# Optimization experiments

Measured on AMD Instinct MI355X. Metric: run time of the kernel, lower is better.

## Reference

```python
import jax, jax.numpy as jnp
import numpy as np

N = 10000        # num_nodes
F_IN = 256       # dataset_num_features
H = 128          # hidden_channels
C_OUT = 40       # dataset_num_classes
L = 3            # num_layers
HEADS = 8
DH = H // HEADS  # per-head dim
E = 160000       # num edges (before self loops)
SCALE = 1.0 / float(np.sqrt(DH))


def setup_inputs() -> dict:
    key = jax.random.key(0)
    ks = jax.random.split(key, 8)
    s = lambda k, *sh: (jax.random.normal(k, sh, dtype=jnp.float32) * 0.05)
    return dict(
        edge_index=jax.random.randint(ks[0], (2, E), 0, N, dtype=jnp.int32),
        x_param=s(ks[1], N, F_IN),
        lin1_w=s(ks[2], F_IN, H),
        lin1_b=jnp.zeros((H,), jnp.float32),
        wq=s(ks[3], L, H, H),
        wk=s(ks[4], L, H, H),
        wv=s(ks[5], L, H, H),
        bq=jnp.zeros((L, H), jnp.float32),
        bk=jnp.zeros((L, H), jnp.float32),
        bv=jnp.zeros((L, H), jnp.float32),
        lin2_w=s(ks[6], H, C_OUT),
        lin2_b=jnp.zeros((C_OUT,), jnp.float32),
    )


def _gcn_norm(edge_index):
    # PyG gcn_norm: add self loops (weight 1), symmetric D^-1/2 A D^-1/2
    loops = jnp.arange(N, dtype=edge_index.dtype)
    row = jnp.concatenate([edge_index[0], loops])  # source j
    col = jnp.concatenate([edge_index[1], loops])  # target i
    deg = jax.ops.segment_sum(jnp.ones(row.shape, jnp.float32), col, num_segments=N)
    dis = jnp.where(deg > 0, jax.lax.rsqrt(jnp.maximum(deg, 1e-12)), 0.0)
    return row, col, dis[row] * dis[col]


def _restricted_softmax(score):
    # softmax with an implicit extra logit at `margin=0`
    m = jnp.maximum(jnp.max(score, axis=-1, keepdims=True), 0.0)
    e = jnp.exp(score - m)
    return e / (jnp.sum(e, axis=-1, keepdims=True) + jnp.exp(-m))


def _forward(edge_index, x_param, lin1_w, lin1_b, wq, wk, wv, bq, bk, bv, lin2_w, lin2_b):
    row, col, norm = _gcn_norm(edge_index)
    # dropouts are eval-mode no-ops
    x = jax.nn.relu(x_param @ lin1_w + lin1_b)  # [N, H]
    x_all = x[:, None, :]                       # [N, 1, H]
    for l in range(L):
        t = x_all.shape[1]
        # project per-node first (linear commutes with per-edge gather)
        q = (x_all[:, -1] @ wq[l] + bq[l]).reshape(N, HEADS, DH)      # query from latest state
        k = (x_all @ wk[l] + bk[l]).reshape(N, t, HEADS, DH)          # keys over full history
        v = (x_all @ wv[l] + bv[l]).reshape(N, t, HEADS, DH)
        qe = q[col]   # [Etot, heads, dh]   (x_i)
        ke = k[row]   # [Etot, t, heads, dh] (x_j)
        ve = v[row]
        score = jnp.einsum('ehd,ethd->eht', qe, ke) * SCALE
        attn = _restricted_softmax(score)        # attention-dropout is a no-op in eval
        msg = jnp.einsum('eht,ethd->ehd', attn, ve).reshape(-1, H) * norm[:, None]
        out = jax.ops.segment_sum(msg, col, num_segments=N)  # aggr='add'
        x = jax.nn.relu(out)
        x_all = jnp.concatenate([x_all, x[:, None, :]], axis=1)
    logits = x_all[:, -1] @ lin2_w + lin2_b
    return jax.nn.log_softmax(logits, axis=1)


def reference(edge_index, x_param, lin1_w, lin1_b, wq, wk, wv, bq, bk, bv, lin2_w, lin2_b):
    return _forward(edge_index, x_param, lin1_w, lin1_b, wq, wk, wv, bq, bk, bv, lin2_w, lin2_b)
```

## Files before the change

kernel.cpp:

```cpp
#include <hip/hip_runtime.h>
#include <math.h>

#define N_NODES 10000
#define F_IN_D  256
#define H_DIM   128
#define C_OUTD  40
#define NHEADS  8
#define NEDGES  160000
#define ETOT    (NEDGES + N_NODES)
#define SCALE_F 0.25f
#define TILES_N 157

typedef __attribute__((ext_vector_type(8))) short bf16x8;
typedef __attribute__((ext_vector_type(4))) float f32x4;
typedef __attribute__((ext_vector_type(2))) float f32x2;

__device__ __forceinline__ unsigned short f2bf(float f) {
    unsigned int u = __float_as_uint(f);
    unsigned int r = (u + 0x7FFFu + ((u >> 16) & 1u)) >> 16;
    return (unsigned short)r;
}
__device__ __forceinline__ float bf2f(unsigned short h) {
    return __uint_as_float(((unsigned int)h) << 16);
}
__device__ __forceinline__ unsigned char f2fp8(float v) {
    int pk = __builtin_amdgcn_cvt_pk_fp8_f32(v, v, 0, false);
    return (unsigned char)(pk & 0xff);
}


__global__ void k_deg_count(const int* __restrict__ col, int* degi) {
    int e = blockIdx.x * 256 + threadIdx.x;
    if (e < NEDGES) atomicAdd(&degi[col[e]], 1);
}

__global__ void k_scan(const int* __restrict__ degi, int* offsets, int* cursor) {
    __shared__ int part[256];
    int tid = threadIdx.x;
    int s = 0;
    if (tid < 250) {
        const int4* d4 = (const int4*)degi;
        for (int i = 0; i < 10; ++i) {
            int4 v = d4[tid * 10 + i];
            s += v.x + v.y + v.z + v.w;
        }
    }
    part[tid] = s;
    __syncthreads();
    for (int off = 1; off < 256; off <<= 1) {
        int v = 0;
        if (tid >= off) v = part[tid - off];
        __syncthreads();
        part[tid] += v;
        __syncthreads();
    }
    if (tid < 250) {
        int base = part[tid] - s;
        int beg = tid * 40;
        for (int i = 0; i < 40; ++i) {
            offsets[beg + i] = base;
            cursor[beg + i]  = 0;
            base += degi[beg + i];
        }
    }
}

__global__ void k_scatter(const int* __restrict__ row, const int* __restrict__ col,
                          const int* __restrict__ degi, const int* __restrict__ offsets,
                          int* cursor, int* csr_row, float* csr_norm) {
    int e = blockIdx.x * 256 + threadIdx.x;
    if (e >= ETOT) return;
    int r, c;
    if (e < NEDGES) { r = row[e]; c = col[e]; }
    else            { r = c = e - NEDGES; }
    int slot = offsets[c] + atomicAdd(&cursor[c], 1);
    float dr = rsqrtf((float)degi[r]);
    float dc = rsqrtf((float)degi[c]);
    csr_row[slot]  = r;
    csr_norm[slot] = dr * dc;
}


__global__ void k_prep(const float* __restrict__ w1, const float* __restrict__ wq,
                       const float* __restrict__ wk, const float* __restrict__ wv,
                       const float* __restrict__ w2,
                       unsigned short* __restrict__ W1T, unsigned short* __restrict__ WTq,
                       unsigned short* __restrict__ WTk, unsigned short* __restrict__ WTv,
                       unsigned short* __restrict__ W2T, int* __restrict__ degi) {
    int b = blockIdx.x;
    if (b < 728) {
        int e = b * 256 + threadIdx.x;
        if (e < 32768) {
            int n = e >> 8, k = e & 255;
            W1T[e] = f2bf(w1[k * H_DIM + n]);
        } else if (e < 180224) {
            int e2 = e - 32768;
            int mat = e2 >> 14;
            int r   = e2 & 16383;
            int n = r >> 7, k = r & 127;
            int l = mat / 3, ws = mat % 3;
            const float*    src = (ws == 0) ? wq  : (ws == 1) ? wk  : wv;
            unsigned short* dst = (ws == 0) ? WTq : (ws == 1) ? WTk : WTv;
            dst[l * 16384 + n * H_DIM + k] = f2bf(src[l * 16384 + k * H_DIM + n]);
        } else if (e < 186368) {
            int e3 = e - 180224;
            int c = e3 >> 7, k = e3 & 127;
            W2T[c * H_DIM + k] = (c < C_OUTD) ? f2bf(w2[k * C_OUTD + c]) : 0;
        }
    } else {
        int i = (b - 728) * 256 + threadIdx.x;
        if (i < N_NODES) degi[i] = 1;
    }
}


__global__ __launch_bounds__(256) void k_lin1_mfma(const float* __restrict__ X,
                                                   const unsigned short* __restrict__ W1T,
                                                   const float* __restrict__ b1,
                                                   unsigned short* __restrict__ X0,
                                                   int nct) {
    int tid = threadIdx.x;
    int wid = tid >> 6, lane = tid & 63;
    int m = lane & 15, quad = lane >> 4;
    int rowA = blockIdx.x * 64 + wid * 16 + m;
    int rowc = rowA < N_NODES ? rowA : N_NODES - 1;
    bf16x8 af[8];
    const float* ap = X + (size_t)rowc * F_IN_D + quad * 8;
    #pragma unroll
    for (int s = 0; s < 8; ++s) {
        float4 lo = *(const float4*)(ap + s * 32);
        float4 hi = *(const float4*)(ap + s * 32 + 4);
        union { unsigned short u[8]; bf16x8 v; } pk;
        pk.u[0] = f2bf(lo.x); pk.u[1] = f2bf(lo.y);
        pk.u[2] = f2bf(lo.z); pk.u[3] = f2bf(lo.w);
        pk.u[4] = f2bf(hi.x); pk.u[5] = f2bf(hi.y);
        pk.u[6] = f2bf(hi.z); pk.u[7] = f2bf(hi.w);
        af[s] = pk.v;
    }
    int row0 = blockIdx.x * 64 + wid * 16 + quad * 4;
    for (int ct = 0; ct < nct; ++ct) {
        int col = ct * 16 + m;
        const unsigned short* bp = W1T + (size_t)col * F_IN_D + quad * 8;
        f32x4 acc = {0.f, 0.f, 0.f, 0.f};
        #pragma unroll
        for (int s = 0; s < 8; ++s) {
            bf16x8 bfr = __builtin_bit_cast(bf16x8, *(const uint4*)(bp + s * 32));
            acc = __builtin_amdgcn_mfma_f32_16x16x32_bf16(af[s], bfr, acc, 0, 0, 0);
        }
        float bb = b1[col];
        #pragma unroll
        for (int rg = 0; rg < 4; ++rg) {
            int r = row0 + rg;
            if (r < N_NODES)
                X0[(size_t)r * H_DIM + col] = f2bf(fmaxf(acc[rg] + bb, 0.f));
        }
    }
}


__global__ __launch_bounds__(256) void k_qkv_mfma(const unsigned short* __restrict__ XHb,
                                                  const unsigned short* __restrict__ WTq,
                                                  const unsigned short* __restrict__ WTk,
                                                  const unsigned short* __restrict__ WTv,
                                                  const float* __restrict__ bq,
                                                  const float* __restrict__ bk,
                                                  const float* __restrict__ bv,
                                                  unsigned short* __restrict__ Qb,
                                                  unsigned char* __restrict__ Kb,
                                                  unsigned char* __restrict__ Vb,
                                                  int l, int t, int nct) {
    int tid = threadIdx.x;
    int wid = tid >> 6, lane = tid & 63;
    int m = lane & 15, quad = lane >> 4;
    int mi = blockIdx.x / TILES_N;
    int rt = blockIdx.x % TILES_N;
    const unsigned short* WT; const float* bias; int slice, mode;
    if (mi == 0)      { WT = WTq; bias = bq; slice = l;          mode = 0; }
    else if (mi <= t) { WT = WTk; bias = bk; slice = mi - 1;     mode = 1; }
    else              { WT = WTv; bias = bv; slice = mi - t - 1; mode = 2; }
    const unsigned short* A = XHb + (size_t)slice * N_NODES * H_DIM;
    int rowA = rt * 64 + wid * 16 + m;
    bf16x8 af[4];
    const unsigned short* ap = A + (size_t)rowA * H_DIM + quad * 8;
    #pragma unroll
    for (int s = 0; s < 4; ++s)
        af[s] = __builtin_bit_cast(bf16x8, *(const uint4*)(ap + s * 32));
    int row0 = rt * 64 + wid * 16 + quad * 4;
    unsigned char* OutB = (mode == 1) ? Kb : Vb;
    for (int cp = 0; cp < nct; ++cp) {
        int colA = cp * 32 + m;
        int colB = colA + 16;
        const unsigned short* bpA = WT + (size_t)colA * H_DIM + quad * 8;
        const unsigned short* bpB = WT + (size_t)colB * H_DIM + quad * 8;
        bf16x8 bA[4], bB[4];
        #pragma unroll
        for (int s = 0; s < 4; ++s) {
            bA[s] = __builtin_bit_cast(bf16x8, *(const uint4*)(bpA + s * 32));
            bB[s] = __builtin_bit_cast(bf16x8, *(const uint4*)(bpB + s * 32));
        }
        f32x4 accA = {0.f, 0.f, 0.f, 0.f};
        f32x4 accB = {0.f, 0.f, 0.f, 0.f};
        #pragma unroll
        for (int s = 0; s < 4; ++s) {
            accA = __builtin_amdgcn_mfma_f32_16x16x32_bf16(af[s], bA[s], accA, 0, 0, 0);
            accB = __builtin_amdgcn_mfma_f32_16x16x32_bf16(af[s], bB[s], accB, 0, 0, 0);
        }
        float bbA = bias[colA], bbB = bias[colB];
        #pragma unroll
        for (int rg = 0; rg < 4; ++rg) {
            int r = row0 + rg;
            if (r < N_NODES) {
                float vA = accA[rg] + bbA;
                float vB = accB[rg] + bbB;
                if (mode == 0) {
                    Qb[(size_t)r * H_DIM + colA] = f2bf(vA);
                    Qb[(size_t)r * H_DIM + colB] = f2bf(vB);
                } else {
                    OutB[((size_t)r * 3 + slice) * H_DIM + colA] = f2fp8(vA);
                    OutB[((size_t)r * 3 + slice) * H_DIM + colB] = f2fp8(vB);
                }
            }
        }
    }
}


template <int T>
__global__ __launch_bounds__(256) void k_attn_agg(const unsigned short* __restrict__ Q,
                                                  const unsigned int* __restrict__ K,
                                                  const unsigned int* __restrict__ V,
                                                  const int* __restrict__ csr_row,
                                                  const float* __restrict__ csr_norm,
                                                  const int* __restrict__ offsets,
                                                  const int* __restrict__ degi,
                                                  unsigned int* __restrict__ Xout) {
    int tid = threadIdx.x;
    int wid = tid >> 6, lane = tid & 63;
    int quarter = lane >> 4, ci = lane & 15;
    int n = blockIdx.x * 4 + wid;
    float q[8];
    {
        uint4 qp = *(const uint4*)&Q[(size_t)n * H_DIM + ci * 8];
        q[0] = __uint_as_float(qp.x << 16) * SCALE_F;
        q[1] = __uint_as_float(qp.x & 0xffff0000u) * SCALE_F;
        q[2] = __uint_as_float(qp.y << 16) * SCALE_F;
        q[3] = __uint_as_float(qp.y & 0xffff0000u) * SCALE_F;
        q[4] = __uint_as_float(qp.z << 16) * SCALE_F;
        q[5] = __uint_as_float(qp.z & 0xffff0000u) * SCALE_F;
        q[6] = __uint_as_float(qp.w << 16) * SCALE_F;
        q[7] = __uint_as_float(qp.w & 0xffff0000u) * SCALE_F;
    }
    int start = offsets[n];
    int cnt   = degi[n];
    int nq = (cnt + 3) >> 2;
    float a[8];
    #pragma unroll
    for (int i = 0; i < 8; ++i) a[i] = 0.f;

    for (int j = 0; j < nq; ++j) {
        int j4 = j * 4 + quarter;
        int valid = j4 < cnt;
        int idx = start + (valid ? j4 : 0);
        int   r   = csr_row[idx];
        float nrm = valid ? csr_norm[idx] : 0.f;
        const uint2* kp = (const uint2*)&K[(size_t)r * 96 + ci * 2];
        const uint2* vp = (const uint2*)&V[(size_t)r * 96 + ci * 2];
        uint2 kw[T], vw[T];
        #pragma unroll
        for (int s = 0; s < T; ++s) { kw[s] = kp[s * 16]; vw[s] = vp[s * 16]; }
        float sc[T];
        #pragma unroll
        for (int s = 0; s < T; ++s) {
            f32x2 k0 = __builtin_amdgcn_cvt_pk_f32_fp8(kw[s].x, false);
            f32x2 k1 = __builtin_amdgcn_cvt_pk_f32_fp8(kw[s].x, true);
            f32x2 k2 = __builtin_amdgcn_cvt_pk_f32_fp8(kw[s].y, false);
            f32x2 k3 = __builtin_amdgcn_cvt_pk_f32_fp8(kw[s].y, true);
            float p = q[0] * k0[0] + q[1] * k0[1] + q[2] * k1[0] + q[3] * k1[1]
                    + q[4] * k2[0] + q[5] * k2[1] + q[6] * k3[0] + q[7] * k3[1];
            p += __shfl_xor(p, 1, 2);
            sc[s] = p;
        }
        float m = 0.f;
        #pragma unroll
        for (int s = 0; s < T; ++s) m = fmaxf(m, sc[s]);
        float den = __expf(-m);
        float mv[8];
        #pragma unroll
        for (int i = 0; i < 8; ++i) mv[i] = 0.f;
        #pragma unroll
        for (int s = 0; s < T; ++s) {
            float w = __expf(sc[s] - m);
            den += w;
            f32x2 v0 = __builtin_amdgcn_cvt_pk_f32_fp8(vw[s].x, false);
            f32x2 v1 = __builtin_amdgcn_cvt_pk_f32_fp8(vw[s].x, true);
            f32x2 v2 = __builtin_amdgcn_cvt_pk_f32_fp8(vw[s].y, false);
            f32x2 v3 = __builtin_amdgcn_cvt_pk_f32_fp8(vw[s].y, true);
            mv[0] += w * v0[0]; mv[1] += w * v0[1];
            mv[2] += w * v1[0]; mv[3] += w * v1[1];
            mv[4] += w * v2[0]; mv[5] += w * v2[1];
            mv[6] += w * v3[0]; mv[7] += w * v3[1];
        }
        float ws = __fdividef(nrm, den);
        #pragma unroll
        for (int i = 0; i < 8; ++i) a[i] += ws * mv[i];
    }
    #pragma unroll
    for (int i = 0; i < 8; ++i) {
        a[i] += __shfl_xor(a[i], 16, 64);
        a[i] += __shfl_xor(a[i], 32, 64);
    }
    if (quarter == 0) {
        uint4 o;
        o.x = ((unsigned int)f2bf(fmaxf(a[1], 0.f)) << 16) | (unsigned int)f2bf(fmaxf(a[0], 0.f));
        o.y = ((unsigned int)f2bf(fmaxf(a[3], 0.f)) << 16) | (unsigned int)f2bf(fmaxf(a[2], 0.f));
        o.z = ((unsigned int)f2bf(fmaxf(a[5], 0.f)) << 16) | (unsigned int)f2bf(fmaxf(a[4], 0.f));
        o.w = ((unsigned int)f2bf(fmaxf(a[7], 0.f)) << 16) | (unsigned int)f2bf(fmaxf(a[6], 0.f));
        *(uint4*)&Xout[(size_t)n * 64 + ci * 4] = o;
    }
}


__global__ __launch_bounds__(256) void k_lin2_mfma(const unsigned short* __restrict__ X,
                                                   const unsigned short* __restrict__ W2T,
                                                   const float* __restrict__ b2,
                                                   float* __restrict__ out) {
    int tid = threadIdx.x;
    int wid = tid >> 6, lane = tid & 63;
    int m = lane & 15, quad = lane >> 4;
    int rowA = blockIdx.x * 64 + wid * 16 + m;
    bf16x8 af[4];
    const unsigned short* ap = X + (size_t)rowA * H_DIM + quad * 8;
    #pragma unroll
    for (int s = 0; s < 4; ++s)
        af[s] = __builtin_bit_cast(bf16x8, *(const uint4*)(ap + s * 32));

    f32x4 acc0 = {0.f, 0.f, 0.f, 0.f};
    f32x4 acc1 = {0.f, 0.f, 0.f, 0.f};
    f32x4 acc2 = {0.f, 0.f, 0.f, 0.f};
    const unsigned short* bp0 = W2T + (size_t)(m)      * H_DIM + quad * 8;
    const unsigned short* bp1 = W2T + (size_t)(16 + m) * H_DIM + quad * 8;
    const unsigned short* bp2 = W2T + (size_t)(32 + m) * H_DIM + quad * 8;
    #pragma unroll
    for (int s = 0; s < 4; ++s) {
        bf16x8 b0 = __builtin_bit_cast(bf16x8, *(const uint4*)(bp0 + s * 32));
        acc0 = __builtin_amdgcn_mfma_f32_16x16x32_bf16(af[s], b0, acc0, 0, 0, 0);
        bf16x8 b1 = __builtin_bit_cast(bf16x8, *(const uint4*)(bp1 + s * 32));
        acc1 = __builtin_amdgcn_mfma_f32_16x16x32_bf16(af[s], b1, acc1, 0, 0, 0);
        bf16x8 b2f = __builtin_bit_cast(bf16x8, *(const uint4*)(bp2 + s * 32));
        acc2 = __builtin_amdgcn_mfma_f32_16x16x32_bf16(af[s], b2f, acc2, 0, 0, 0);
    }

    float bb0 = b2[m], bb1 = b2[16 + m];
    float bb2 = (m < 8) ? b2[32 + m] : 0.f;
    int row0 = blockIdx.x * 64 + wid * 16 + quad * 4;
    #pragma unroll
    for (int rg = 0; rg < 4; ++rg) {
        int r = row0 + rg;
        float v0 = acc0[rg] + bb0;
        float v1 = acc1[rg] + bb1;
        float v2 = (m < 8) ? (acc2[rg] + bb2) : -INFINITY;
        float mx = fmaxf(fmaxf(v0, v1), v2);
        #pragma unroll
        for (int o = 8; o > 0; o >>= 1) mx = fmaxf(mx, __shfl_xor(mx, o, 16));
        float sm = __expf(v0 - mx) + __expf(v1 - mx) + ((m < 8) ? __expf(v2 - mx) : 0.f);
        #pragma unroll
        for (int o = 8; o > 0; o >>= 1) sm += __shfl_xor(sm, o, 16);
        float lse = mx + __logf(sm);
        if (r < N_NODES) {
            out[(size_t)r * C_OUTD + m]      = v0 - lse;
            out[(size_t)r * C_OUTD + 16 + m] = v1 - lse;
            if (m < 8) out[(size_t)r * C_OUTD + 32 + m] = v2 - lse;
        }
    }
}


extern "C" void kernel_launch(void* const* d_in, const int* in_sizes, int n_in,
                              void* d_out, int out_size, void* d_ws, size_t ws_size,
                              hipStream_t stream) {
    const int*   ei      = (const int*)d_in[0];
    const int*   row     = ei;
    const int*   col     = ei + NEDGES;
    const float* x_param = (const float*)d_in[1];
    const float* lin1_w  = (const float*)d_in[2];
    const float* lin1_b  = (const float*)d_in[3];
    const float* wq      = (const float*)d_in[4];
    const float* wk      = (const float*)d_in[5];
    const float* wv      = (const float*)d_in[6];
    const float* bq      = (const float*)d_in[7];
    const float* bk      = (const float*)d_in[8];
    const float* bv      = (const float*)d_in[9];
    const float* lin2_w  = (const float*)d_in[10];
    const float* lin2_b  = (const float*)d_in[11];
    float*       out     = (float*)d_out;

    char* wbase = (char*)d_ws;
    size_t off = 0;
    auto alloc = [&](size_t bytes) -> void* {
        off = (off + 255) & ~(size_t)255;
        void* p = wbase + off;
        off += bytes;
        return p;
    };
    int*            degi     = (int*)           alloc((size_t)N_NODES * 4);
    int*            offsets  = (int*)           alloc((size_t)N_NODES * 4);
    int*            cursor   = (int*)           alloc((size_t)N_NODES * 4);
    int*            csr_row  = (int*)           alloc((size_t)ETOT * 4);
    float*          csr_norm = (float*)         alloc((size_t)ETOT * 4);
    unsigned short* W1T      = (unsigned short*)alloc((size_t)H_DIM * F_IN_D * 2);
    unsigned short* WTq      = (unsigned short*)alloc((size_t)3 * H_DIM * H_DIM * 2);
    unsigned short* WTk      = (unsigned short*)alloc((size_t)3 * H_DIM * H_DIM * 2);
    unsigned short* WTv      = (unsigned short*)alloc((size_t)3 * H_DIM * H_DIM * 2);
    unsigned short* W2T      = (unsigned short*)alloc((size_t)48 * H_DIM * 2);
    unsigned short* XHb      = (unsigned short*)alloc((size_t)4 * N_NODES * H_DIM * 2);
    unsigned short* Qb       = (unsigned short*)alloc((size_t)N_NODES * H_DIM * 2);
    unsigned char*  Kb       = (unsigned char*) alloc((size_t)N_NODES * 3 * H_DIM);
    unsigned char*  Vb       = (unsigned char*) alloc((size_t)N_NODES * 3 * H_DIM);

    k_prep<<<768, 256, 0, stream>>>(lin1_w, wq, wk, wv, lin2_w,
                                    W1T, WTq, WTk, WTv, W2T, degi);
    k_deg_count<<<(NEDGES + 255) / 256, 256, 0, stream>>>(col, degi);
    k_scan     <<<1, 256, 0, stream>>>(degi, offsets, cursor);
    k_scatter  <<<(ETOT + 255) / 256, 256, 0, stream>>>(row, col, degi, offsets, cursor,
                                                        csr_row, csr_norm);

    k_lin1_mfma<<<TILES_N, 256, 0, stream>>>(x_param, W1T, lin1_b, XHb, 8);

    for (int l = 0; l < 3; ++l) {
        int t = l + 1;
        k_qkv_mfma<<<(1 + 2 * t) * TILES_N, 256, 0, stream>>>(
            XHb, WTq + (size_t)l * 16384, WTk + (size_t)l * 16384, WTv + (size_t)l * 16384,
            bq + l * H_DIM, bk + l * H_DIM, bv + l * H_DIM,
            Qb, Kb, Vb, l, t, 4);
        unsigned int* Xnext = (unsigned int*)(XHb + (size_t)(l + 1) * N_NODES * H_DIM);
        if (t == 1)
            k_attn_agg<1><<<2500, 256, 0, stream>>>(Qb, (const unsigned int*)Kb,
                                                    (const unsigned int*)Vb, csr_row,
                                                    csr_norm, offsets, degi, Xnext);
        else if (t == 2)
            k_attn_agg<2><<<2500, 256, 0, stream>>>(Qb, (const unsigned int*)Kb,
                                                    (const unsigned int*)Vb, csr_row,
                                                    csr_norm, offsets, degi, Xnext);
        else
            k_attn_agg<3><<<2500, 256, 0, stream>>>(Qb, (const unsigned int*)Kb,
                                                    (const unsigned int*)Vb, csr_row,
                                                    csr_norm, offsets, degi, Xnext);
    }

    k_lin2_mfma<<<TILES_N, 256, 0, stream>>>(XHb + (size_t)3 * N_NODES * H_DIM,
                                             W2T, lin2_b, out);
}
```

Before: 258.9 us.

## Fuse K/V projections per block and fold lin2+log_softmax into last attention

The QKV kernel now computes K and V for the same history slice in one block, so the A-fragment loads of X are shared and the grid shrinks from (1+2t) to (1+t) tile groups. The final attention layer also computes the lin2 projection and log_softmax in-kernel via shared memory, which removes the separate lin2 launch and the write-back and reload of the last hidden state. In exchange, lin2 now runs on scalar FMAs with per-lane weight rows instead of MFMA, and each K/V block does twice the column work.

```diff
diff --git a/kernel.cpp b/kernel.cpp
--- a/kernel.cpp
+++ b/kernel.cpp
@@ -168,16 +168,13 @@
                                                   unsigned short* __restrict__ Qb,
                                                   unsigned char* __restrict__ Kb,
                                                   unsigned char* __restrict__ Vb,
-                                                  int l, int t, int nct) {
+                                                  int l, int t, int nq) {
     int tid = threadIdx.x;
     int wid = tid >> 6, lane = tid & 63;
     int m = lane & 15, quad = lane >> 4;
     int mi = blockIdx.x / TILES_N;
     int rt = blockIdx.x % TILES_N;
-    const unsigned short* WT; const float* bias; int slice, mode;
-    if (mi == 0)      { WT = WTq; bias = bq; slice = l;          mode = 0; }
-    else if (mi <= t) { WT = WTk; bias = bk; slice = mi - 1;     mode = 1; }
-    else              { WT = WTv; bias = bv; slice = mi - t - 1; mode = 2; }
+    int slice = (mi == 0) ? l : (mi - 1);
     const unsigned short* A = XHb + (size_t)slice * N_NODES * H_DIM;
     int rowA = rt * 64 + wid * 16 + m;
     bf16x8 af[4];
@@ -186,46 +183,71 @@
     for (int s = 0; s < 4; ++s)
         af[s] = __builtin_bit_cast(bf16x8, *(const uint4*)(ap + s * 32));
     int row0 = rt * 64 + wid * 16 + quad * 4;
-    unsigned char* OutB = (mode == 1) ? Kb : Vb;
-    for (int cp = 0; cp < nct; ++cp) {
-        int colA = cp * 32 + m;
-        int colB = colA + 16;
-        const unsigned short* bpA = WT + (size_t)colA * H_DIM + quad * 8;
-        const unsigned short* bpB = WT + (size_t)colB * H_DIM + quad * 8;
-        bf16x8 bA[4], bB[4];
-        #pragma unroll
-        for (int s = 0; s < 4; ++s) {
-            bA[s] = __builtin_bit_cast(bf16x8, *(const uint4*)(bpA + s * 32));
-            bB[s] = __builtin_bit_cast(bf16x8, *(const uint4*)(bpB + s * 32));
-        }
-        f32x4 accA = {0.f, 0.f, 0.f, 0.f};
-        f32x4 accB = {0.f, 0.f, 0.f, 0.f};
-        #pragma unroll
-        for (int s = 0; s < 4; ++s) {
-            accA = __builtin_amdgcn_mfma_f32_16x16x32_bf16(af[s], bA[s], accA, 0, 0, 0);
-            accB = __builtin_amdgcn_mfma_f32_16x16x32_bf16(af[s], bB[s], accB, 0, 0, 0);
-        }
-        float bbA = bias[colA], bbB = bias[colB];
-        #pragma unroll
-        for (int rg = 0; rg < 4; ++rg) {
-            int r = row0 + rg;
-            if (r < N_NODES) {
-                float vA = accA[rg] + bbA;
-                float vB = accB[rg] + bbB;
-                if (mode == 0) {
-                    Qb[(size_t)r * H_DIM + colA] = f2bf(vA);
-                    Qb[(size_t)r * H_DIM + colB] = f2bf(vB);
-                } else {
-                    OutB[((size_t)r * 3 + slice) * H_DIM + colA] = f2fp8(vA);
-                    OutB[((size_t)r * 3 + slice) * H_DIM + colB] = f2fp8(vB);
+
+    if (mi == 0) {
+        for (int cp = 0; cp < nq; ++cp) {
+            int colA = cp * 32 + m;
+            int colB = colA + 16;
+            const unsigned short* bpA = WTq + (size_t)colA * H_DIM + quad * 8;
+            const unsigned short* bpB = WTq + (size_t)colB * H_DIM + quad * 8;
+            bf16x8 bA[4], bB[4];
+            #pragma unroll
+            for (int s = 0; s < 4; ++s) {
+                bA[s] = __builtin_bit_cast(bf16x8, *(const uint4*)(bpA + s * 32));
+                bB[s] = __builtin_bit_cast(bf16x8, *(const uint4*)(bpB + s * 32));
+            }
+            f32x4 accA = {0.f, 0.f, 0.f, 0.f};
+            f32x4 accB = {0.f, 0.f, 0.f, 0.f};
+            #pragma unroll
+            for (int s = 0; s < 4; ++s) {
+                accA = __builtin_amdgcn_mfma_f32_16x16x32_bf16(af[s], bA[s], accA, 0, 0, 0);
+                accB = __builtin_amdgcn_mfma_f32_16x16x32_bf16(af[s], bB[s], accB, 0, 0, 0);
+            }
+            float bbA = bq[colA], bbB = bq[colB];
+            #pragma unroll
+            for (int rg = 0; rg < 4; ++rg) {
+                int r = row0 + rg;
+                if (r < N_NODES) {
+                    Qb[(size_t)r * H_DIM + colA] = f2bf(accA[rg] + bbA);
+                    Qb[(size_t)r * H_DIM + colB] = f2bf(accB[rg] + bbB);
                 }
             }
         }
-    }
-}
-
-
-template <int T>
+    } else {
+        int ncols = 2 * nq;
+        for (int ct = 0; ct < ncols; ++ct) {
+            int col = ct * 16 + m;
+            const unsigned short* bpK = WTk + (size_t)col * H_DIM + quad * 8;
+            const unsigned short* bpV = WTv + (size_t)col * H_DIM + quad * 8;
+            bf16x8 bK[4], bV[4];
+            #pragma unroll
+            for (int s = 0; s < 4; ++s) {
+                bK[s] = __builtin_bit_cast(bf16x8, *(const uint4*)(bpK + s * 32));
+                bV[s] = __builtin_bit_cast(bf16x8, *(const uint4*)(bpV + s * 32));
+            }
+            f32x4 accK = {0.f, 0.f, 0.f, 0.f};
+            f32x4 accV = {0.f, 0.f, 0.f, 0.f};
+            #pragma unroll
+            for (int s = 0; s < 4; ++s) {
+                accK = __builtin_amdgcn_mfma_f32_16x16x32_bf16(af[s], bK[s], accK, 0, 0, 0);
+                accV = __builtin_amdgcn_mfma_f32_16x16x32_bf16(af[s], bV[s], accV, 0, 0, 0);
+            }
+            float bbK = bk[col], bbV = bv[col];
+            #pragma unroll
+            for (int rg = 0; rg < 4; ++rg) {
+                int r = row0 + rg;
+                if (r < N_NODES) {
+                    size_t base = ((size_t)r * 3 + slice) * H_DIM + col;
+                    Kb[base] = f2fp8(accK[rg] + bbK);
+                    Vb[base] = f2fp8(accV[rg] + bbV);
+                }
+            }
+        }
+    }
+}
+
+
+template <int T, bool L2F>
 __global__ __launch_bounds__(256) void k_attn_agg(const unsigned short* __restrict__ Q,
                                                   const unsigned int* __restrict__ K,
                                                   const unsigned int* __restrict__ V,
@@ -233,7 +255,11 @@
                                                   const float* __restrict__ csr_norm,
                                                   const int* __restrict__ offsets,
                                                   const int* __restrict__ degi,
-                                                  unsigned int* __restrict__ Xout) {
+                                                  unsigned int* __restrict__ Xout,
+                                                  const unsigned short* __restrict__ W2T,
+                                                  const float* __restrict__ b2,
+                                                  float* __restrict__ out) {
+    __shared__ float xrow[4][128];
     int tid = threadIdx.x;
     int wid = tid >> 6, lane = tid & 63;
     int quarter = lane >> 4, ci = lane & 15;
@@ -309,68 +335,50 @@
         a[i] += __shfl_xor(a[i], 16, 64);
         a[i] += __shfl_xor(a[i], 32, 64);
     }
-    if (quarter == 0) {
-        uint4 o;
-        o.x = ((unsigned int)f2bf(fmaxf(a[1], 0.f)) << 16) | (unsigned int)f2bf(fmaxf(a[0], 0.f));
-        o.y = ((unsigned int)f2bf(fmaxf(a[3], 0.f)) << 16) | (unsigned int)f2bf(fmaxf(a[2], 0.f));
-        o.z = ((unsigned int)f2bf(fmaxf(a[5], 0.f)) << 16) | (unsigned int)f2bf(fmaxf(a[4], 0.f));
-        o.w = ((unsigned int)f2bf(fmaxf(a[7], 0.f)) << 16) | (unsigned int)f2bf(fmaxf(a[6], 0.f));
-        *(uint4*)&Xout[(size_t)n * 64 + ci * 4] = o;
-    }
-}
-
-
-__global__ __launch_bounds__(256) void k_lin2_mfma(const unsigned short* __restrict__ X,
-                                                   const unsigned short* __restrict__ W2T,
-                                                   const float* __restrict__ b2,
-                                                   float* __restrict__ out) {
-    int tid = threadIdx.x;
-    int wid = tid >> 6, lane = tid & 63;
-    int m = lane & 15, quad = lane >> 4;
-    int rowA = blockIdx.x * 64 + wid * 16 + m;
-    bf16x8 af[4];
-    const unsigned short* ap = X + (size_t)rowA * H_DIM + quad * 8;
-    #pragma unroll
-    for (int s = 0; s < 4; ++s)
-        af[s] = __builtin_bit_cast(bf16x8, *(const uint4*)(ap + s * 32));
-
-    f32x4 acc0 = {0.f, 0.f, 0.f, 0.f};
-    f32x4 acc1 = {0.f, 0.f, 0.f, 0.f};
-    f32x4 acc2 = {0.f, 0.f, 0.f, 0.f};
-    const unsigned short* bp0 = W2T + (size_t)(m)      * H_DIM + quad * 8;
-    const unsigned short* bp1 = W2T + (size_t)(16 + m) * H_DIM + quad * 8;
-    const unsigned short* bp2 = W2T + (size_t)(32 + m) * H_DIM + quad * 8;
-    #pragma unroll
-    for (int s = 0; s < 4; ++s) {
-        bf16x8 b0 = __builtin_bit_cast(bf16x8, *(const uint4*)(bp0 + s * 32));
-        acc0 = __builtin_amdgcn_mfma_f32_16x16x32_bf16(af[s], b0, acc0, 0, 0, 0);
-        bf16x8 b1 = __builtin_bit_cast(bf16x8, *(const uint4*)(bp1 + s * 32));
-        acc1 = __builtin_amdgcn_mfma_f32_16x16x32_bf16(af[s], b1, acc1, 0, 0, 0);
-        bf16x8 b2f = __builtin_bit_cast(bf16x8, *(const uint4*)(bp2 + s * 32));
-        acc2 = __builtin_amdgcn_mfma_f32_16x16x32_bf16(af[s], b2f, acc2, 0, 0, 0);
-    }
-
-    float bb0 = b2[m], bb1 = b2[16 + m];
-    float bb2 = (m < 8) ? b2[32 + m] : 0.f;
-    int row0 = blockIdx.x * 64 + wid * 16 + quad * 4;
-    #pragma unroll
-    for (int rg = 0; rg < 4; ++rg) {
-        int r = row0 + rg;
-        float v0 = acc0[rg] + bb0;
-        float v1 = acc1[rg] + bb1;
-        float v2 = (m < 8) ? (acc2[rg] + bb2) : -INFINITY;
-        float mx = fmaxf(fmaxf(v0, v1), v2);
-        #pragma unroll
-        for (int o = 8; o > 0; o >>= 1) mx = fmaxf(mx, __shfl_xor(mx, o, 16));
-        float sm = __expf(v0 - mx) + __expf(v1 - mx) + ((m < 8) ? __expf(v2 - mx) : 0.f);
-        #pragma unroll
-        for (int o = 8; o > 0; o >>= 1) sm += __shfl_xor(sm, o, 16);
+
+    if (!L2F) {
+        if (quarter == 0) {
+            uint4 o;
+            o.x = ((unsigned int)f2bf(fmaxf(a[1], 0.f)) << 16) | (unsigned int)f2bf(fmaxf(a[0], 0.f));
+            o.y = ((unsigned int)f2bf(fmaxf(a[3], 0.f)) << 16) | (unsigned int)f2bf(fmaxf(a[2], 0.f));
+            o.z = ((unsigned int)f2bf(fmaxf(a[5], 0.f)) << 16) | (unsigned int)f2bf(fmaxf(a[4], 0.f));
+            o.w = ((unsigned int)f2bf(fmaxf(a[7], 0.f)) << 16) | (unsigned int)f2bf(fmaxf(a[6], 0.f));
+            *(uint4*)&Xout[(size_t)n * 64 + ci * 4] = o;
+        }
+    } else {
+        if (quarter == 0) {
+            #pragma unroll
+            for (int i = 0; i < 8; ++i) xrow[wid][ci * 8 + i] = fmaxf(a[i], 0.f);
+        }
+        __syncthreads();
+        const float* xr = xrow[wid];
+        int c = lane;
+        int cw = (c < 48) ? c : 0;
+        const unsigned short* wr = W2T + (size_t)cw * H_DIM;
+        float acc = (c < C_OUTD) ? b2[c] : 0.f;
+        for (int k0 = 0; k0 < H_DIM; k0 += 8) {
+            uint4 wv4 = *(const uint4*)(wr + k0);
+            float4 x0 = *(const float4*)&xr[k0];
+            float4 x1 = *(const float4*)&xr[k0 + 4];
+            acc += x0.x * __uint_as_float(wv4.x << 16)
+                 + x0.y * __uint_as_float(wv4.x & 0xffff0000u)
+                 + x0.z * __uint_as_float(wv4.y << 16)
+                 + x0.w * __uint_as_float(wv4.y & 0xffff0000u)
+                 + x1.x * __uint_as_float(wv4.z << 16)
+                 + x1.y * __uint_as_float(wv4.z & 0xffff0000u)
+                 + x1.z * __uint_as_float(wv4.w << 16)
+                 + x1.w * __uint_as_float(wv4.w & 0xffff0000u);
+        }
+        float lg = (c < C_OUTD) ? acc : -INFINITY;
+        float mx = lg;
+        #pragma unroll
+        for (int o = 32; o > 0; o >>= 1) mx = fmaxf(mx, __shfl_xor(mx, o, 64));
+        float e = (c < C_OUTD) ? __expf(lg - mx) : 0.f;
+        float sm = e;
+        #pragma unroll
+        for (int o = 32; o > 0; o >>= 1) sm += __shfl_xor(sm, o, 64);
         float lse = mx + __logf(sm);
-        if (r < N_NODES) {
-            out[(size_t)r * C_OUTD + m]      = v0 - lse;
-            out[(size_t)r * C_OUTD + 16 + m] = v1 - lse;
-            if (m < 8) out[(size_t)r * C_OUTD + 32 + m] = v2 - lse;
-        }
+        if (c < C_OUTD) out[(size_t)n * C_OUTD + c] = lg - lse;
     }
 }
 
@@ -428,25 +436,22 @@
 
     for (int l = 0; l < 3; ++l) {
         int t = l + 1;
-        k_qkv_mfma<<<(1 + 2 * t) * TILES_N, 256, 0, stream>>>(
+        k_qkv_mfma<<<(1 + t) * TILES_N, 256, 0, stream>>>(
             XHb, WTq + (size_t)l * 16384, WTk + (size_t)l * 16384, WTv + (size_t)l * 16384,
             bq + l * H_DIM, bk + l * H_DIM, bv + l * H_DIM,
             Qb, Kb, Vb, l, t, 4);
         unsigned int* Xnext = (unsigned int*)(XHb + (size_t)(l + 1) * N_NODES * H_DIM);
         if (t == 1)
-            k_attn_agg<1><<<2500, 256, 0, stream>>>(Qb, (const unsigned int*)Kb,
-                                                    (const unsigned int*)Vb, csr_row,
-                                                    csr_norm, offsets, degi, Xnext);
+            k_attn_agg<1, false><<<2500, 256, 0, stream>>>(
+                Qb, (const unsigned int*)Kb, (const unsigned int*)Vb, csr_row,
+                csr_norm, offsets, degi, Xnext, W2T, lin2_b, out);
         else if (t == 2)
-            k_attn_agg<2><<<2500, 256, 0, stream>>>(Qb, (const unsigned int*)Kb,
-                                                    (const unsigned int*)Vb, csr_row,
-                                                    csr_norm, offsets, degi, Xnext);
+            k_attn_agg<2, false><<<2500, 256, 0, stream>>>(
+                Qb, (const unsigned int*)Kb, (const unsigned int*)Vb, csr_row,
+                csr_norm, offsets, degi, Xnext, W2T, lin2_b, out);
         else
-            k_attn_agg<3><<<2500, 256, 0, stream>>>(Qb, (const unsigned int*)Kb,
-                                                    (const unsigned int*)Vb, csr_row,
-                                                    csr_norm, offsets, degi, Xnext);
-    }
-
-    k_lin2_mfma<<<TILES_N, 256, 0, stream>>>(XHb + (size_t)3 * N_NODES * H_DIM,
-                                             W2T, lin2_b, out);
-}
+            k_attn_agg<3, true><<<2500, 256, 0, stream>>>(
+                Qb, (const unsigned int*)Kb, (const unsigned int*)Vb, csr_row,
+                csr_norm, offsets, degi, Xnext, W2T, lin2_b, out);
+    }
+}
```

After: 275.6 us. 6.5% more time.
